# Kernel tuning notes

Hardware: AMD Instinct MI355X
Metric: run time of the kernel (lower is better)

The kernel has to match this reference:

```python
import jax, jax.numpy as jnp
import numpy as np

DIM = 1536
NHEADS = 24
HEAD_DIM = DIM // NHEADS
EPS = 1e-6


def rms_norm(x):
    # normalize over last dim, no learned weight
    ms = jnp.mean(x * x, axis=-1, keepdims=True)
    return x * jax.lax.rsqrt(ms + EPS)


def rope_non_neox(x, cos, sin):
    # x: [B, S, H, D]; cos/sin: [S, D] -> broadcast [1, S, 1, D]
    # non-neox (GPT-J / interleaved) style: pairs are (x0,x1),(x2,x3),...
    c = cos[None, :, None, :]
    s = sin[None, :, None, :]
    x1 = x[..., 0::2]
    x2 = x[..., 1::2]
    c1 = c[..., 0::2]
    s1 = s[..., 0::2]
    o1 = x1 * c1 - x2 * s1
    o2 = x2 * c1 + x1 * s1
    out = jnp.stack([o1, o2], axis=-1).reshape(x.shape)
    return out


def setup_inputs() -> dict:
    key = jax.random.key(0)
    k1, k2, k3, k4, k5 = jax.random.split(key, 5)
    B, S = 4, 4096
    x = jax.random.normal(k1, (B, S, DIM), dtype=jnp.float32)
    # rotary tables: build valid cos/sin from random angles (interleaved duplication)
    half = HEAD_DIM // 2
    inv_freq = 1.0 / (10000.0 ** (jnp.arange(0, half, dtype=jnp.float32) / half))
    t = jnp.arange(S, dtype=jnp.float32)
    freqs = jnp.outer(t, inv_freq)  # [S, D/2]
    cos = jnp.repeat(jnp.cos(freqs), 2, axis=-1)  # [S, D] interleaved
    sin = jnp.repeat(jnp.sin(freqs), 2, axis=-1)
    w_qkv = jax.random.normal(k2, (DIM, 3 * DIM), dtype=jnp.float32) * (DIM ** -0.5)
    b_qkv = jax.random.normal(k3, (3 * DIM,), dtype=jnp.float32) * 0.02
    return {"x": x, "cos": cos, "sin": sin, "w_qkv": w_qkv, "b_qkv": b_qkv}


def reference(x, cos, sin, w_qkv, b_qkv):
    B, S, _ = x.shape
    H, D = NHEADS, HEAD_DIM
    qkv = jnp.einsum('bsd,de->bse', x, w_qkv) + b_qkv  # [B,S,3*DIM]
    q, k, v = jnp.split(qkv, 3, axis=-1)
    q = q.reshape(B, S, H, D)
    k = k.reshape(B, S, H, D)
    v = v.reshape(B, S, H, D)
    q = rms_norm(q)
    k = rms_norm(k)
    q = rope_non_neox(q, cos, sin)
    k = rope_non_neox(k, cos, sin)
    # SDPA: [B,H,S,D]
    qh = q.transpose(0, 2, 1, 3)
    kh = k.transpose(0, 2, 1, 3)
    vh = v.transpose(0, 2, 1, 3)
    scale = D ** -0.5
    scores = jnp.einsum('bhqd,bhkd->bhqk', qh, kh) * scale
    attn = jax.nn.softmax(scores, axis=-1)
    out = jnp.einsum('bhqk,bhkd->bhqd', attn, vh)
    out = out.transpose(0, 2, 1, 3).reshape(B, S, H * D)
    return out
```

## Files before the change

### kernel.cpp

```cpp
#include <hip/hip_runtime.h>

#define DIM   1536
#define NQKV  4608
#define NH    24
#define HD    64
#define BATCH 4
#define SEQ   4096
#define ROWS  16384

typedef _Float16 f16x8 __attribute__((ext_vector_type(8)));
typedef float    f32x4 __attribute__((ext_vector_type(4)));

__device__ __forceinline__ void gload_lds16(const void* g, void* l) {
  __builtin_amdgcn_global_load_lds(
      (const __attribute__((address_space(1))) unsigned int*)g,
      (__attribute__((address_space(3))) unsigned int*)l, 16, 0, 0);
}
__device__ __forceinline__ float fexp2(float x) {
#if __has_builtin(__builtin_amdgcn_exp2f)
  return __builtin_amdgcn_exp2f(x);
#else
  return exp2f(x);
#endif
}

#define QSCALE 0.18033688011112042f

__global__ __launch_bounds__(256) void convert_x(const float* __restrict__ X,
                                                 _Float16* __restrict__ Xh) {
  const int i = (blockIdx.x * 256 + threadIdx.x) * 8;
  float4 a = *(const float4*)(X + i);
  float4 b = *(const float4*)(X + i + 4);
  f16x8 h;
  h[0] = (_Float16)a.x; h[1] = (_Float16)a.y; h[2] = (_Float16)a.z; h[3] = (_Float16)a.w;
  h[4] = (_Float16)b.x; h[5] = (_Float16)b.y; h[6] = (_Float16)b.z; h[7] = (_Float16)b.w;
  *(f16x8*)(Xh + i) = h;
}

__global__ __launch_bounds__(256) void transpose_w(const float* __restrict__ W,
                                                   _Float16* __restrict__ Wt) {
  __shared__ float tile[32][33];
  const int tx = threadIdx.x, ty = threadIdx.y;
  const int k0 = blockIdx.y * 32, n0 = blockIdx.x * 32;
  #pragma unroll
  for (int i = 0; i < 32; i += 8)
    tile[ty + i][tx] = W[(size_t)(k0 + ty + i) * NQKV + n0 + tx];
  __syncthreads();
  #pragma unroll
  for (int i = 0; i < 32; i += 8)
    Wt[(size_t)(n0 + ty + i) * DIM + k0 + tx] = (_Float16)tile[tx][ty + i];
}

__global__ __launch_bounds__(256) void qkv_gemm(const _Float16* __restrict__ Xh,
                                                const _Float16* __restrict__ Wt,
                                                const float* __restrict__ Bias,
                                                const float* __restrict__ Cos,
                                                const float* __restrict__ Sin,
                                                _Float16* __restrict__ QKV) {
  __shared__ _Float16 As[128 * 64];
  __shared__ _Float16 Bs[128 * 64];
  const int w    = threadIdx.x >> 6;
  const int lane = threadIdx.x & 63;
  const int lr   = lane >> 3, lc = lane & 7;
  const int quad = lane >> 4, l15 = lane & 15;
  const int m0 = blockIdx.y * 128;
  const int n0 = blockIdx.x * 128;
  const int waveR = (w >> 1) * 64;
  const int waveC = (w & 1) * 64;

  f32x4 acc[4][4];
  #pragma unroll
  for (int i = 0; i < 4; i++)
    #pragma unroll
    for (int j = 0; j < 4; j++) acc[i][j] = (f32x4){0.f, 0.f, 0.f, 0.f};

  for (int kt = 0; kt < DIM / 64; ++kt) {
    const int k0 = kt * 64;
    #pragma unroll
    for (int i = 0; i < 4; ++i) {
      const int rr = w * 32 + i * 8;
      gload_lds16(Xh + (size_t)(m0 + rr + lr) * DIM + k0 + lc * 8, &As[rr * 64]);
      gload_lds16(Wt + (size_t)(n0 + rr + lr) * DIM + k0 + lc * 8, &Bs[rr * 64]);
    }
    __syncthreads();
    #pragma unroll
    for (int ks = 0; ks < 2; ++ks) {
      f16x8 aF[4], bF[4];
      #pragma unroll
      for (int t = 0; t < 4; t++)
        aF[t] = *(const f16x8*)&As[(waveR + t * 16 + l15) * 64 + ks * 32 + quad * 8];
      #pragma unroll
      for (int t = 0; t < 4; t++)
        bF[t] = *(const f16x8*)&Bs[(waveC + t * 16 + l15) * 64 + ks * 32 + quad * 8];
      #pragma unroll
      for (int mt = 0; mt < 4; mt++)
        #pragma unroll
        for (int nt = 0; nt < 4; nt++)
          acc[mt][nt] = __builtin_amdgcn_mfma_f32_16x16x32_f16(aF[mt], bF[nt], acc[mt][nt], 0, 0, 0);
    }
    __syncthreads();
  }

  const int nCol0  = n0 + waveC;
  const int region = nCol0 / DIM;

  float bias[4];
  #pragma unroll
  for (int nt = 0; nt < 4; nt++) bias[nt] = Bias[nCol0 + nt * 16 + l15];

  if (region == 2) {
    #pragma unroll
    for (int nt = 0; nt < 4; nt++) {
      const int n = nCol0 + nt * 16 + l15;
      #pragma unroll
      for (int mt = 0; mt < 4; mt++) {
        const int mBase = m0 + waveR + mt * 16 + quad * 4;
        #pragma unroll
        for (int r = 0; r < 4; r++)
          QKV[(size_t)(mBase + r) * NQKV + n] = (_Float16)(acc[mt][nt][r] + bias[nt]);
      }
    }
  } else {
    const float qsc = (region == 0) ? QSCALE : 1.0f;
    #pragma unroll
    for (int mt = 0; mt < 4; mt++) {
      const int mBase = m0 + waveR + mt * 16 + quad * 4;
      #pragma unroll
      for (int r = 0; r < 4; r++) {
        const int m = mBase + r;
        const int s = m & (SEQ - 1);
        float v[4];
        float ss = 0.f;
        #pragma unroll
        for (int nt = 0; nt < 4; nt++) {
          v[nt] = acc[mt][nt][r] + bias[nt];
          ss += v[nt] * v[nt];
        }
        #pragma unroll
        for (int off = 1; off < 16; off <<= 1) ss += __shfl_xor(ss, off);
        const float rinv = rsqrtf(ss * (1.f / 64.f) + 1e-6f);
        #pragma unroll
        for (int nt = 0; nt < 4; nt++) {
          const int d = nt * 16 + l15;
          const float c  = Cos[s * HD + d];
          const float si = Sin[s * HD + d];
          const float x  = v[nt] * rinv;
          const float xp = __shfl_xor(x, 1);
          float o = (l15 & 1) ? (x * c + xp * si) : (x * c - xp * si);
          o *= qsc;
          QKV[(size_t)m * NQKV + nCol0 + d] = (_Float16)o;
        }
      }
    }
  }
}

#define LSTR 72
#define NBLK (SEQ / 128 * BATCH * NH)
__global__ __launch_bounds__(256) void flash_attn(const _Float16* __restrict__ QKV,
                                                  float* __restrict__ Out) {
  __shared__ __align__(16) _Float16 sm[2 * 64 * LSTR + 4 * 32 * LSTR];
  _Float16* Ks  = sm;
  _Float16* Vts = sm + 64 * LSTR;
  const int w = threadIdx.x >> 6;
  _Float16* Ps = sm + 2 * 64 * LSTR + w * 32 * LSTR;
  const int lane = threadIdx.x & 63;
  const int quad = lane >> 4, l15 = lane & 15;
  const int Lraw = blockIdx.x;
  const int swz  = (Lraw & 7) * (NBLK / 8) + (Lraw >> 3);
  const int qt = swz & 31;
  const int bh = swz >> 5;
  const int b  = bh / NH;
  const int h  = bh - b * NH;
  const size_t rowb = (size_t)b * SEQ * NQKV + (size_t)h * HD;

  f16x8 qreg[2][2];
  #pragma unroll
  for (int mt = 0; mt < 2; mt++)
    #pragma unroll
    for (int ks = 0; ks < 2; ks++) {
      const int row = qt * 128 + w * 32 + mt * 16 + l15;
      qreg[mt][ks] = *(const f16x8*)(QKV + rowb + (size_t)row * NQKV + ks * 32 + quad * 8);
    }

  f16x8 onesF;
  {
    const _Float16 one = (_Float16)(l15 == 0 ? 1.0f : 0.0f);
    #pragma unroll
    for (int j = 0; j < 8; j++) onesF[j] = one;
  }

  f32x4 o[2][4], o4[2];
  #pragma unroll
  for (int mt = 0; mt < 2; mt++) {
    o4[mt] = (f32x4){0.f, 0.f, 0.f, 0.f};
    #pragma unroll
    for (int t = 0; t < 4; t++) o[mt][t] = (f32x4){0.f, 0.f, 0.f, 0.f};
  }

  for (int kt = 0; kt < SEQ / 64; ++kt) {
    __syncthreads();
    #pragma unroll
    for (int i = 0; i < 2; i++) {
      const int chunk = threadIdx.x + i * 256;
      const int r = chunk >> 3, c0 = (chunk & 7) * 8;
      *(uint4*)&Ks[r * LSTR + c0] =
          *(const uint4*)(QKV + rowb + (size_t)(kt * 64 + r) * NQKV + DIM + c0);
    }
    #pragma unroll
    for (int i = 0; i < 2; i++) {
      const int c0 = w * 16 + i * 8;
      union { uint4 v; _Float16 u[8]; } d;
      d.v = *(const uint4*)(QKV + rowb + (size_t)(kt * 64 + lane) * NQKV + 2 * DIM + c0);
      #pragma unroll
      for (int j = 0; j < 8; j++) Vts[(c0 + j) * LSTR + lane] = d.u[j];
    }
    __syncthreads();

    f32x4 sacc[2][4];
    #pragma unroll
    for (int mt = 0; mt < 2; mt++)
      #pragma unroll
      for (int t = 0; t < 4; t++) sacc[mt][t] = (f32x4){0.f, 0.f, 0.f, 0.f};
    #pragma unroll
    for (int ks = 0; ks < 2; ks++) {
      f16x8 bF[4];
      #pragma unroll
      for (int t = 0; t < 4; t++)
        bF[t] = *(const f16x8*)&Ks[(t * 16 + l15) * LSTR + ks * 32 + quad * 8];
      #pragma unroll
      for (int mt = 0; mt < 2; mt++)
        #pragma unroll
        for (int t = 0; t < 4; t++)
          sacc[mt][t] = __builtin_amdgcn_mfma_f32_16x16x32_f16(qreg[mt][ks], bF[t], sacc[mt][t], 0, 0, 0);
    }

    #pragma unroll
    for (int mt = 0; mt < 2; mt++)
      #pragma unroll
      for (int t = 0; t < 4; t++)
        #pragma unroll
        for (int r = 0; r < 4; r++) {
          const _Float16 ph = (_Float16)fexp2(sacc[mt][t][r]);
          Ps[(mt * 16 + quad * 4 + r) * LSTR + t * 16 + l15] = ph;
        }

    #pragma unroll
    for (int ks = 0; ks < 2; ks++) {
      f16x8 pF[2];
      #pragma unroll
      for (int mt = 0; mt < 2; mt++)
        pF[mt] = *(const f16x8*)&Ps[(mt * 16 + l15) * LSTR + ks * 32 + quad * 8];
      #pragma unroll
      for (int t = 0; t < 4; t++) {
        f16x8 vF = *(const f16x8*)&Vts[(t * 16 + l15) * LSTR + ks * 32 + quad * 8];
        #pragma unroll
        for (int mt = 0; mt < 2; mt++)
          o[mt][t] = __builtin_amdgcn_mfma_f32_16x16x32_f16(pF[mt], vF, o[mt][t], 0, 0, 0);
      }
      #pragma unroll
      for (int mt = 0; mt < 2; mt++)
        o4[mt] = __builtin_amdgcn_mfma_f32_16x16x32_f16(pF[mt], onesF, o4[mt], 0, 0, 0);
    }
  }

  #pragma unroll
  for (int mt = 0; mt < 2; mt++) {
    float lrow[4];
    #pragma unroll
    for (int r = 0; r < 4; r++) lrow[r] = __shfl(o4[mt][r], lane & 48);
    #pragma unroll
    for (int t = 0; t < 4; t++)
      #pragma unroll
      for (int r = 0; r < 4; r++) {
        const int srow = qt * 128 + w * 32 + mt * 16 + quad * 4 + r;
        const int d = t * 16 + l15;
        Out[((size_t)(b * SEQ + srow)) * DIM + h * HD + d] = o[mt][t][r] / lrow[r];
      }
  }
}

extern "C" void kernel_launch(void* const* d_in, const int* in_sizes, int n_in,
                              void* d_out, int out_size, void* d_ws, size_t ws_size,
                              hipStream_t stream) {
  const float* X    = (const float*)d_in[0];
  const float* Cos  = (const float*)d_in[1];
  const float* Sin  = (const float*)d_in[2];
  const float* W    = (const float*)d_in[3];
  const float* Bias = (const float*)d_in[4];
  float* Out = (float*)d_out;

  char* ws = (char*)d_ws;
  _Float16* Xh  = (_Float16*)(ws);
  _Float16* Wt  = (_Float16*)(ws + 50331648);
  _Float16* QKV = (_Float16*)(ws + 64487424);

  convert_x  <<<dim3(ROWS * DIM / (8 * 256)), 256, 0, stream>>>(X, Xh);
  transpose_w<<<dim3(NQKV / 32, DIM / 32), dim3(32, 8), 0, stream>>>(W, Wt);
  qkv_gemm   <<<dim3(NQKV / 128, ROWS / 128), 256, 0, stream>>>(Xh, Wt, Bias, Cos, Sin, QKV);
  flash_attn <<<dim3(NBLK), 256, 0, stream>>>(QKV, Out);
}
```

Baseline: 1.318 ms.

## Compute S transposed with 32x32 MFMA and feed P to PV via permlane swap

```diff
diff --git a/kernel.cpp b/kernel.cpp
--- a/kernel.cpp
+++ b/kernel.cpp
@@ -9,7 +9,10 @@
 #define ROWS  16384
 
 typedef _Float16 f16x8 __attribute__((ext_vector_type(8)));
+typedef _Float16 f16x2 __attribute__((ext_vector_type(2)));
 typedef float    f32x4 __attribute__((ext_vector_type(4)));
+typedef float    f32x16 __attribute__((ext_vector_type(16)));
+typedef unsigned u32x2 __attribute__((ext_vector_type(2)));
 
 __device__ __forceinline__ void gload_lds16(const void* g, void* l) {
   __builtin_amdgcn_global_load_lds(
@@ -21,6 +24,20 @@
   return __builtin_amdgcn_exp2f(x);
 #else
   return exp2f(x);
+#endif
+}
+
+__device__ __forceinline__ void swap32(unsigned& a, unsigned& b) {
+#if __has_builtin(__builtin_amdgcn_permlane32_swap)
+  u32x2 r = __builtin_amdgcn_permlane32_swap(a, b, false, false);
+  a = r[0]; b = r[1];
+#else
+  const int hi = (threadIdx.x & 63) >> 5;
+  unsigned as = (unsigned)__shfl_xor((int)a, 32);
+  unsigned bs = (unsigned)__shfl_xor((int)b, 32);
+  unsigned na = hi ? bs : a;
+  unsigned nb = hi ? b  : as;
+  a = na; b = nb;
 #endif
 }
 
@@ -156,47 +173,31 @@
 }
 
 #define LSTR 72
-#define NBLK (SEQ / 128 * BATCH * NH)
 __global__ __launch_bounds__(256) void flash_attn(const _Float16* __restrict__ QKV,
                                                   float* __restrict__ Out) {
-  __shared__ __align__(16) _Float16 sm[2 * 64 * LSTR + 4 * 32 * LSTR];
+  __shared__ __align__(16) _Float16 sm[2 * 64 * LSTR];
   _Float16* Ks  = sm;
   _Float16* Vts = sm + 64 * LSTR;
-  const int w = threadIdx.x >> 6;
-  _Float16* Ps = sm + 2 * 64 * LSTR + w * 32 * LSTR;
+  const int w    = threadIdx.x >> 6;
   const int lane = threadIdx.x & 63;
-  const int quad = lane >> 4, l15 = lane & 15;
-  const int Lraw = blockIdx.x;
-  const int swz  = (Lraw & 7) * (NBLK / 8) + (Lraw >> 3);
-  const int qt = swz & 31;
-  const int bh = swz >> 5;
+  const int l31  = lane & 31;
+  const int hi   = lane >> 5;
+  const int qt = blockIdx.x;
+  const int bh = blockIdx.y;
   const int b  = bh / NH;
   const int h  = bh - b * NH;
   const size_t rowb = (size_t)b * SEQ * NQKV + (size_t)h * HD;
 
-  f16x8 qreg[2][2];
-  #pragma unroll
-  for (int mt = 0; mt < 2; mt++)
-    #pragma unroll
-    for (int ks = 0; ks < 2; ks++) {
-      const int row = qt * 128 + w * 32 + mt * 16 + l15;
-      qreg[mt][ks] = *(const f16x8*)(QKV + rowb + (size_t)row * NQKV + ks * 32 + quad * 8);
-    }
-
-  f16x8 onesF;
+  f16x8 qreg[4];
   {
-    const _Float16 one = (_Float16)(l15 == 0 ? 1.0f : 0.0f);
-    #pragma unroll
-    for (int j = 0; j < 8; j++) onesF[j] = one;
-  }
-
-  f32x4 o[2][4], o4[2];
-  #pragma unroll
-  for (int mt = 0; mt < 2; mt++) {
-    o4[mt] = (f32x4){0.f, 0.f, 0.f, 0.f};
-    #pragma unroll
-    for (int t = 0; t < 4; t++) o[mt][t] = (f32x4){0.f, 0.f, 0.f, 0.f};
-  }
+    const int row = qt * 128 + w * 32 + l31;
+    #pragma unroll
+    for (int dw = 0; dw < 4; dw++)
+      qreg[dw] = *(const f16x8*)(QKV + rowb + (size_t)row * NQKV + dw * 16 + hi * 8);
+  }
+
+  f32x16 o[2] = {};
+  float lsum = 0.f;
 
   for (int kt = 0; kt < SEQ / 64; ++kt) {
     __syncthreads();
@@ -217,66 +218,55 @@
     }
     __syncthreads();
 
-    f32x4 sacc[2][4];
-    #pragma unroll
-    for (int mt = 0; mt < 2; mt++)
-      #pragma unroll
-      for (int t = 0; t < 4; t++) sacc[mt][t] = (f32x4){0.f, 0.f, 0.f, 0.f};
-    #pragma unroll
-    for (int ks = 0; ks < 2; ks++) {
-      f16x8 bF[4];
-      #pragma unroll
-      for (int t = 0; t < 4; t++)
-        bF[t] = *(const f16x8*)&Ks[(t * 16 + l15) * LSTR + ks * 32 + quad * 8];
-      #pragma unroll
-      for (int mt = 0; mt < 2; mt++)
-        #pragma unroll
-        for (int t = 0; t < 4; t++)
-          sacc[mt][t] = __builtin_amdgcn_mfma_f32_16x16x32_f16(qreg[mt][ks], bF[t], sacc[mt][t], 0, 0, 0);
-    }
-
-    #pragma unroll
-    for (int mt = 0; mt < 2; mt++)
-      #pragma unroll
-      for (int t = 0; t < 4; t++)
-        #pragma unroll
-        for (int r = 0; r < 4; r++) {
-          const _Float16 ph = (_Float16)fexp2(sacc[mt][t][r]);
-          Ps[(mt * 16 + quad * 4 + r) * LSTR + t * 16 + l15] = ph;
+    #pragma unroll
+    for (int kt32 = 0; kt32 < 2; ++kt32) {
+      f32x16 sacc = {};
+      #pragma unroll
+      for (int dw = 0; dw < 4; dw++) {
+        f16x8 kF = *(const f16x8*)&Ks[(kt32 * 32 + l31) * LSTR + dw * 16 + hi * 8];
+        sacc = __builtin_amdgcn_mfma_f32_32x32x16_f16(kF, qreg[dw], sacc, 0, 0, 0);
+      }
+
+      unsigned pk[8];
+      #pragma unroll
+      for (int i = 0; i < 8; i++) {
+        union { f16x2 h2; unsigned u; } uu;
+        uu.h2[0] = (_Float16)fexp2(sacc[2 * i]);
+        uu.h2[1] = (_Float16)fexp2(sacc[2 * i + 1]);
+        lsum += (float)uu.h2[0] + (float)uu.h2[1];
+        pk[i] = uu.u;
+      }
+      swap32(pk[0], pk[2]);
+      swap32(pk[1], pk[3]);
+      swap32(pk[4], pk[6]);
+      swap32(pk[5], pk[7]);
+
+      #pragma unroll
+      for (int h16 = 0; h16 < 2; ++h16) {
+        const int kw = kt32 * 2 + h16;
+        union { unsigned u[4]; f16x8 f; } pa;
+        pa.u[0] = pk[h16 * 4 + 0];
+        pa.u[1] = pk[h16 * 4 + 1];
+        pa.u[2] = pk[h16 * 4 + 2];
+        pa.u[3] = pk[h16 * 4 + 3];
+        #pragma unroll
+        for (int dt = 0; dt < 2; ++dt) {
+          f16x8 vF = *(const f16x8*)&Vts[(dt * 32 + l31) * LSTR + kw * 16 + hi * 8];
+          o[dt] = __builtin_amdgcn_mfma_f32_32x32x16_f16(pa.f, vF, o[dt], 0, 0, 0);
         }
-
-    #pragma unroll
-    for (int ks = 0; ks < 2; ks++) {
-      f16x8 pF[2];
-      #pragma unroll
-      for (int mt = 0; mt < 2; mt++)
-        pF[mt] = *(const f16x8*)&Ps[(mt * 16 + l15) * LSTR + ks * 32 + quad * 8];
-      #pragma unroll
-      for (int t = 0; t < 4; t++) {
-        f16x8 vF = *(const f16x8*)&Vts[(t * 16 + l15) * LSTR + ks * 32 + quad * 8];
-        #pragma unroll
-        for (int mt = 0; mt < 2; mt++)
-          o[mt][t] = __builtin_amdgcn_mfma_f32_16x16x32_f16(pF[mt], vF, o[mt][t], 0, 0, 0);
-      }
-      #pragma unroll
-      for (int mt = 0; mt < 2; mt++)
-        o4[mt] = __builtin_amdgcn_mfma_f32_16x16x32_f16(pF[mt], onesF, o4[mt], 0, 0, 0);
-    }
-  }
-
-  #pragma unroll
-  for (int mt = 0; mt < 2; mt++) {
-    float lrow[4];
-    #pragma unroll
-    for (int r = 0; r < 4; r++) lrow[r] = __shfl(o4[mt][r], lane & 48);
-    #pragma unroll
-    for (int t = 0; t < 4; t++)
-      #pragma unroll
-      for (int r = 0; r < 4; r++) {
-        const int srow = qt * 128 + w * 32 + mt * 16 + quad * 4 + r;
-        const int d = t * 16 + l15;
-        Out[((size_t)(b * SEQ + srow)) * DIM + h * HD + d] = o[mt][t][r] / lrow[r];
-      }
+      }
+    }
+  }
+
+  const float ls = lsum + __shfl_xor(lsum, 32);
+  #pragma unroll
+  for (int r = 0; r < 16; r++) {
+    const int q = (r & 3) + 8 * (r >> 2) + 4 * hi;
+    const float lrow = __shfl(ls, q);
+    const int srow = qt * 128 + w * 32 + q;
+    #pragma unroll
+    for (int dt = 0; dt < 2; dt++)
+      Out[((size_t)(b * SEQ + srow)) * DIM + h * HD + dt * 32 + l31] = o[dt][r] / lrow;
   }
 }
 
@@ -298,5 +288,5 @@
   convert_x  <<<dim3(ROWS * DIM / (8 * 256)), 256, 0, stream>>>(X, Xh);
   transpose_w<<<dim3(NQKV / 32, DIM / 32), dim3(32, 8), 0, stream>>>(W, Wt);
   qkv_gemm   <<<dim3(NQKV / 128, ROWS / 128), 256, 0, stream>>>(Xh, Wt, Bias, Cos, Sin, QKV);
-  flash_attn <<<dim3(NBLK), 256, 0, stream>>>(QKV, Out);
-}
+  flash_attn <<<dim3(SEQ / 128, BATCH * NH), 256, 0, stream>>>(QKV, Out);
+}
```

Result: faster. 1.110 ms (-15.8%).
